# Kernel optimization log

Measured on AMD Instinct MI355X. Metric: run time of the kernel, lower is better.

## Reference

```python
import jax, jax.numpy as jnp
import numpy as np

N_NODES = 10000
N_EDGES = 160000
D = 512
DROPOUT_P = 0.5
NEG_SLOPE = 0.25


def setup_inputs() -> dict:
    key = jax.random.key(0)
    ks = jax.random.split(key, 8)
    H = jax.random.normal(ks[0], (N_NODES, D), dtype=jnp.float32)
    rows = jax.random.randint(ks[1], (N_EDGES,), 0, N_NODES)
    cols = jax.random.randint(ks[2], (N_EDGES,), 0, N_NODES)
    vals = jax.random.uniform(ks[3], (N_EDGES,), dtype=jnp.float32)
    # xavier-normal-ish weights, zero bias (matches torch init)
    std = float(np.sqrt(2.0 / (D + D)))
    W1 = jax.random.normal(ks[4], (D, D), dtype=jnp.float32) * std
    b1 = jnp.zeros((D,), dtype=jnp.float32)
    W2 = jax.random.normal(ks[5], (D, D), dtype=jnp.float32) * std
    b2 = jnp.zeros((D,), dtype=jnp.float32)
    return {"H": H, "rows": rows, "cols": cols, "vals": vals,
            "W1": W1, "b1": b1, "W2": W2, "b2": b2}


def _spmm(rows, cols, vals, dense):
    # sparse [N,N] @ dense [N,D] via gather + segment-sum
    gathered = vals[:, None] * dense[cols]          # [E, D]
    return jax.ops.segment_sum(gathered, rows, num_segments=N_NODES)


def _leaky_relu(x):
    return jnp.where(x >= 0, x, NEG_SLOPE * x)


def reference(H, rows, cols, vals, W1, b1, W2, b2):
    # layer 1: dense GEMM -> SpMM -> bias -> leaky_relu -> dropout(training=True)
    h = _spmm(rows, cols, vals, H @ W1) + b1
    h = _leaky_relu(h)
    keep = jax.random.bernoulli(jax.random.key(42), 1.0 - DROPOUT_P, h.shape)
    h = jnp.where(keep, h / (1.0 - DROPOUT_P), 0.0)
    # layer 2
    h = _spmm(rows, cols, vals, h @ W2) + b2
    return _leaky_relu(h)
```

## Files before the change

kernel.cpp:

```cpp
#include <hip/hip_runtime.h>
#include <stdint.h>

#define N_NODES 10000
#define M_PAD   10112
#define N_EDGES 160000
#define DIM     512
#define N_ELEMS 5120000
#define NEG_SLOPE 0.25f
#define ELL_W   64

typedef short          short8   __attribute__((ext_vector_type(8)));
typedef unsigned short ushort8v __attribute__((ext_vector_type(8)));
typedef __bf16         bf16x8   __attribute__((ext_vector_type(8)));
typedef float          f32x4    __attribute__((ext_vector_type(4)));

__device__ __forceinline__ unsigned short f2bf(float f) {
    uint32_t u = __builtin_bit_cast(uint32_t, f);
    uint32_t r = (u + 0x7fffu + ((u >> 16) & 1u)) >> 16;
    return (unsigned short)r;
}
__device__ __forceinline__ float b2f(unsigned short u) {
    return __builtin_bit_cast(float, (uint32_t)u << 16);
}

__device__ __forceinline__ uint32_t rotl32(uint32_t x, uint32_t d) {
    return (x << d) | (x >> (32u - d));
}
__device__ __forceinline__ void threefry_42(uint32_t x0, uint32_t x1,
                                            uint32_t& o0, uint32_t& o1) {
    const uint32_t ks0 = 0u, ks1 = 42u, ks2 = 0x1BD11BDAu ^ 42u;
    x0 += ks0; x1 += ks1;
#define TF_R4(a,b,c,d) \
    x0 += x1; x1 = rotl32(x1,a); x1 ^= x0; \
    x0 += x1; x1 = rotl32(x1,b); x1 ^= x0; \
    x0 += x1; x1 = rotl32(x1,c); x1 ^= x0; \
    x0 += x1; x1 = rotl32(x1,d); x1 ^= x0;
    TF_R4(13,15,26,6);  x0 += ks1; x1 += ks2 + 1u;
    TF_R4(17,29,16,24); x0 += ks2; x1 += ks0 + 2u;
    TF_R4(13,15,26,6);  x0 += ks0; x1 += ks1 + 3u;
    TF_R4(17,29,16,24); x0 += ks1; x1 += ks2 + 4u;
    TF_R4(13,15,26,6);  x0 += ks2; x1 += ks0 + 5u;
#undef TF_R4
    o0 = x0; o1 = x1;
}

#define CONV_BLKS 5000
#define TR_BLKS   64
#define EZ_BLKS   1250
#define ZERO_BLKS 10

__device__ __forceinline__ void transpose_tile(const float* __restrict__ W,
                                               unsigned short* __restrict__ WT,
                                               int tile, float (*ts)[65]) {
    int k0 = (tile & 7) * 64, n0 = (tile >> 3) * 64;
    int tx = threadIdx.x & 15, ty = threadIdx.x >> 4;
    #pragma unroll
    for (int i = 0; i < 4; ++i) {
        int k = i * 16 + ty;
        float4 v = *(const float4*)&W[(size_t)(k0 + k) * DIM + n0 + tx * 4];
        ts[k][tx * 4 + 0] = v.x; ts[k][tx * 4 + 1] = v.y;
        ts[k][tx * 4 + 2] = v.z; ts[k][tx * 4 + 3] = v.w;
    }
    __syncthreads();
    #pragma unroll
    for (int i = 0; i < 4; ++i) {
        int n = i * 16 + ty;
        ushort4 o;
        o.x = f2bf(ts[tx * 4 + 0][n]); o.y = f2bf(ts[tx * 4 + 1][n]);
        o.z = f2bf(ts[tx * 4 + 2][n]); o.w = f2bf(ts[tx * 4 + 3][n]);
        *(ushort4*)&WT[(size_t)(n0 + n) * DIM + k0 + tx * 4] = o;
    }
}

__global__ __launch_bounds__(256)
void prep_kernel(const float* __restrict__ H, const float* __restrict__ W1,
                 const float* __restrict__ W2, unsigned short* __restrict__ Abf,
                 unsigned short* __restrict__ WT1, unsigned short* __restrict__ WT2,
                 int4* __restrict__ epack4, int* __restrict__ deg) {
    __shared__ float ts[64][65];
    int b = blockIdx.x;
    if (b < CONV_BLKS) {
        int i = b * 256 + threadIdx.x;
        float4 v = ((const float4*)H)[i];
        ushort4 o;
        o.x = f2bf(v.x); o.y = f2bf(v.y); o.z = f2bf(v.z); o.w = f2bf(v.w);
        ((ushort4*)Abf)[i] = o;
    } else if (b < CONV_BLKS + TR_BLKS) {
        transpose_tile(W1, WT1, b - CONV_BLKS, ts);
    } else if (b < CONV_BLKS + 2 * TR_BLKS) {
        transpose_tile(W2, WT2, b - CONV_BLKS - TR_BLKS, ts);
    } else if (b < CONV_BLKS + 2 * TR_BLKS + EZ_BLKS) {
        int i = (b - CONV_BLKS - 2 * TR_BLKS) * 256 + threadIdx.x;
        epack4[i] = make_int4(0, 0, 0, 0);
    } else {
        int i = (b - CONV_BLKS - 2 * TR_BLKS - EZ_BLKS) * 1024 + threadIdx.x * 4;
        #pragma unroll
        for (int j = 0; j < 4; ++j)
            if (i + j < N_NODES) deg[i + j] = 0;
    }
}

__global__ void ell_scatter(const int* __restrict__ rows, const int* __restrict__ cols,
                            const float* __restrict__ vals, int* __restrict__ deg,
                            int2* __restrict__ epack) {
    int e = blockIdx.x * blockDim.x + threadIdx.x;
    if (e < N_EDGES) {
        int r = rows[e];
        int p = atomicAdd(&deg[r], 1);
        epack[(size_t)r * ELL_W + p] = make_int2(cols[e], __float_as_int(vals[e]));
    }
}

__global__ __launch_bounds__(256)
void mfma_gemm(const unsigned short* __restrict__ A, const unsigned short* __restrict__ BT,
               unsigned short* __restrict__ C, int M) {
    __shared__ short8 As[1024];
    __shared__ short8 Bs[1024];
    int tid  = threadIdx.x;
    int wid  = tid >> 6, lane = tid & 63;
    int bm   = blockIdx.x * 128;
    int bn   = blockIdx.y * 128;
    int wm   = (wid >> 1) * 64, wn = (wid & 1) * 64;

    f32x4 acc[4][4] = {};
    int srow = lane >> 3;
    int sslot = lane & 7;

    for (int k0 = 0; k0 < DIM; k0 += 64) {
        #pragma unroll
        for (int c = 0; c < 4; ++c) {
            int chunk = wid * 4 + c;
            int r  = chunk * 8 + srow;
            int ks = sslot ^ (r & 7);
            const unsigned short* ga = A  + (size_t)(bm + r) * DIM + k0 + ks * 8;
            const unsigned short* gb = BT + (size_t)(bn + r) * DIM + k0 + ks * 8;
            __builtin_amdgcn_global_load_lds(
                (const __attribute__((address_space(1))) void*)ga,
                (__attribute__((address_space(3))) void*)&As[chunk * 64], 16, 0, 0);
            __builtin_amdgcn_global_load_lds(
                (const __attribute__((address_space(1))) void*)gb,
                (__attribute__((address_space(3))) void*)&Bs[chunk * 64], 16, 0, 0);
        }
        __syncthreads();

        int lrow = lane & 15;
        int kgrp = lane >> 4;
        #pragma unroll
        for (int ks = 0; ks < 2; ++ks) {
            short8 af[4], bfr[4];
            #pragma unroll
            for (int i = 0; i < 4; ++i) {
                int r = wm + i * 16 + lrow;
                af[i]  = As[r * 8 + ((ks * 4 + kgrp) ^ (r & 7))];
                int n = wn + i * 16 + lrow;
                bfr[i] = Bs[n * 8 + ((ks * 4 + kgrp) ^ (n & 7))];
            }
            #pragma unroll
            for (int i = 0; i < 4; ++i)
                #pragma unroll
                for (int j = 0; j < 4; ++j)
                    acc[i][j] = __builtin_amdgcn_mfma_f32_16x16x32_bf16(
                        __builtin_bit_cast(bf16x8, af[i]),
                        __builtin_bit_cast(bf16x8, bfr[j]), acc[i][j], 0, 0, 0);
        }
        __syncthreads();
    }

    int crow = (lane >> 4) * 4;
    int ccol = lane & 15;
    #pragma unroll
    for (int i = 0; i < 4; ++i) {
        #pragma unroll
        for (int r = 0; r < 4; ++r) {
            int row = bm + wm + i * 16 + crow + r;
            if (row < M) {
                size_t base = (size_t)row * DIM + bn + wn + ccol;
                #pragma unroll
                for (int j = 0; j < 4; ++j)
                    C[base + j * 16] = f2bf(acc[i][j][r]);
            }
        }
    }
}

#define ACC2(v, U) \
    acc0 = fmaf(v, __builtin_bit_cast(float, (U) << 16), acc0); \
    acc1 = fmaf(v, __builtin_bit_cast(float, (U) & 0xffff0000u), acc1);

template <int LAYER>
__global__ __launch_bounds__(256)
void spmm_kernel(const unsigned short* __restrict__ X, const int* __restrict__ deg,
                 const int2* __restrict__ epack, const float* __restrict__ bias,
                 void* __restrict__ outp) {
    int b    = blockIdx.x;
    int q    = (b & 7) >> 1;
    int pi   = ((b >> 3) << 1) | (b & 1);
    int row  = pi * 4 + (threadIdx.x >> 6);
    int lane = threadIdx.x & 63;
    int d  = deg[row];
    int dp = (d + 7) & ~7;
    const int2* ep = epack + (size_t)row * ELL_W;
    const uint32_t* X2 = (const uint32_t*)X;
    uint32_t qoff = q * 64 + lane;

    float acc0 = 0.f, acc1 = 0.f;
    int base = 0;
    for (; base + 16 <= dp; base += 16) {
        int4 eA = *(const int4*)(ep + base);
        int4 eB = *(const int4*)(ep + base + 2);
        int4 eC = *(const int4*)(ep + base + 4);
        int4 eD = *(const int4*)(ep + base + 6);
        int4 eE = *(const int4*)(ep + base + 8);
        int4 eF = *(const int4*)(ep + base + 10);
        int4 eG = *(const int4*)(ep + base + 12);
        int4 eH = *(const int4*)(ep + base + 14);
        uint32_t x0 = X2[(size_t)eA.x * 256 + qoff];
        uint32_t x1 = X2[(size_t)eA.z * 256 + qoff];
        uint32_t x2 = X2[(size_t)eB.x * 256 + qoff];
        uint32_t x3 = X2[(size_t)eB.z * 256 + qoff];
        uint32_t x4 = X2[(size_t)eC.x * 256 + qoff];
        uint32_t x5 = X2[(size_t)eC.z * 256 + qoff];
        uint32_t x6 = X2[(size_t)eD.x * 256 + qoff];
        uint32_t x7 = X2[(size_t)eD.z * 256 + qoff];
        uint32_t x8 = X2[(size_t)eE.x * 256 + qoff];
        uint32_t x9 = X2[(size_t)eE.z * 256 + qoff];
        uint32_t xa = X2[(size_t)eF.x * 256 + qoff];
        uint32_t xb = X2[(size_t)eF.z * 256 + qoff];
        uint32_t xc = X2[(size_t)eG.x * 256 + qoff];
        uint32_t xd = X2[(size_t)eG.z * 256 + qoff];
        uint32_t xe = X2[(size_t)eH.x * 256 + qoff];
        uint32_t xf = X2[(size_t)eH.z * 256 + qoff];
        float v0 = __int_as_float(eA.y), v1 = __int_as_float(eA.w);
        float v2 = __int_as_float(eB.y), v3 = __int_as_float(eB.w);
        float v4 = __int_as_float(eC.y), v5 = __int_as_float(eC.w);
        float v6 = __int_as_float(eD.y), v7 = __int_as_float(eD.w);
        float v8 = __int_as_float(eE.y), v9 = __int_as_float(eE.w);
        float va = __int_as_float(eF.y), vb = __int_as_float(eF.w);
        float vc = __int_as_float(eG.y), vd = __int_as_float(eG.w);
        float ve = __int_as_float(eH.y), vf = __int_as_float(eH.w);
        ACC2(v0, x0) ACC2(v1, x1) ACC2(v2, x2) ACC2(v3, x3)
        ACC2(v4, x4) ACC2(v5, x5) ACC2(v6, x6) ACC2(v7, x7)
        ACC2(v8, x8) ACC2(v9, x9) ACC2(va, xa) ACC2(vb, xb)
        ACC2(vc, xc) ACC2(vd, xd) ACC2(ve, xe) ACC2(vf, xf)
    }
    if (base < dp) {
        int4 eA = *(const int4*)(ep + base);
        int4 eB = *(const int4*)(ep + base + 2);
        int4 eC = *(const int4*)(ep + base + 4);
        int4 eD = *(const int4*)(ep + base + 6);
        uint32_t x0 = X2[(size_t)eA.x * 256 + qoff];
        uint32_t x1 = X2[(size_t)eA.z * 256 + qoff];
        uint32_t x2 = X2[(size_t)eB.x * 256 + qoff];
        uint32_t x3 = X2[(size_t)eB.z * 256 + qoff];
        uint32_t x4 = X2[(size_t)eC.x * 256 + qoff];
        uint32_t x5 = X2[(size_t)eC.z * 256 + qoff];
        uint32_t x6 = X2[(size_t)eD.x * 256 + qoff];
        uint32_t x7 = X2[(size_t)eD.z * 256 + qoff];
        float v0 = __int_as_float(eA.y), v1 = __int_as_float(eA.w);
        float v2 = __int_as_float(eB.y), v3 = __int_as_float(eB.w);
        float v4 = __int_as_float(eC.y), v5 = __int_as_float(eC.w);
        float v6 = __int_as_float(eD.y), v7 = __int_as_float(eD.w);
        ACC2(v0, x0) ACC2(v1, x1) ACC2(v2, x2) ACC2(v3, x3)
        ACC2(v4, x4) ACC2(v5, x5) ACC2(v6, x6) ACC2(v7, x7)
    }

    float2 bi = ((const float2*)bias)[q * 64 + lane];
    float r0 = acc0 + bi.x, r1 = acc1 + bi.y;
    r0 = (r0 >= 0.f) ? r0 : NEG_SLOPE * r0;
    r1 = (r1 >= 0.f) ? r1 : NEG_SLOPE * r1;
    if (LAYER == 1) {
        uint32_t e0 = (uint32_t)row * DIM + q * 128 + lane * 2;
        uint32_t o0, o1;
        threefry_42(0u, e0, o0, o1);
        uint32_t bits0 = o0 ^ o1;
        threefry_42(0u, e0 + 1, o0, o1);
        uint32_t bits1 = o0 ^ o1;
        float w0 = ((int)bits0 >= 0) ? r0 * 2.0f : 0.0f;
        float w1 = ((int)bits1 >= 0) ? r1 * 2.0f : 0.0f;
        uint32_t o = (uint32_t)f2bf(w0) | ((uint32_t)f2bf(w1) << 16);
        ((uint32_t*)outp)[(size_t)row * 256 + q * 64 + lane] = o;
    } else {
        float2 o = make_float2(r0, r1);
        ((float2*)outp)[(size_t)row * 256 + q * 64 + lane] = o;
    }
}

extern "C" void kernel_launch(void* const* d_in, const int* in_sizes, int n_in,
                              void* d_out, int out_size, void* d_ws, size_t ws_size,
                              hipStream_t stream) {
    const float* H    = (const float*)d_in[0];
    const int*   rows = (const int*)  d_in[1];
    const int*   cols = (const int*)  d_in[2];
    const float* vals = (const float*)d_in[3];
    const float* W1   = (const float*)d_in[4];
    const float* b1   = (const float*)d_in[5];
    const float* W2   = (const float*)d_in[6];
    const float* b2   = (const float*)d_in[7];
    float* out = (float*)d_out;

    char* ws = (char*)d_ws;
    size_t off = 0;
    auto alloc = [&](size_t bytes) -> void* {
        off = (off + 255) & ~(size_t)255;
        void* p = ws + off;
        off += bytes;
        return p;
    };
    int*  deg   = (int*) alloc((size_t)N_NODES * 4);
    int2* epack = (int2*)alloc((size_t)N_NODES * ELL_W * 8);
    unsigned short* WT1 = (unsigned short*)alloc((size_t)DIM * DIM * 2);
    unsigned short* WT2 = (unsigned short*)alloc((size_t)DIM * DIM * 2);
    unsigned short* Abf = (unsigned short*)alloc((size_t)M_PAD * DIM * 2);
    unsigned short* hbf = (unsigned short*)alloc((size_t)M_PAD * DIM * 2);
    unsigned short* Xbf = (unsigned short*)alloc((size_t)N_NODES * DIM * 2);

    int prep_blocks = CONV_BLKS + 2 * TR_BLKS + EZ_BLKS + ZERO_BLKS;
    prep_kernel<<<prep_blocks, 256, 0, stream>>>(H, W1, W2, Abf, WT1, WT2,
                                                 (int4*)epack, deg);
    ell_scatter<<<(N_EDGES + 255) / 256, 256, 0, stream>>>(rows, cols, vals, deg, epack);

    dim3 ggrid(M_PAD / 128, DIM / 128);
    mfma_gemm<<<ggrid, 256, 0, stream>>>(Abf, WT1, Xbf, N_NODES);
    spmm_kernel<1><<<N_NODES, 256, 0, stream>>>(Xbf, deg, epack, b1, hbf);
    mfma_gemm<<<ggrid, 256, 0, stream>>>(hbf, WT2, Xbf, N_NODES);
    spmm_kernel<2><<<N_NODES, 256, 0, stream>>>(Xbf, deg, epack, b2, out);
}
```

Baseline: 104.3 us.

## Assign SpMM work items per XCD via atomic queues for L2 locality

Replaces the static block-to-(row group, column quarter) mapping in the SpMM kernels with dynamic work fetching. Each block reads its XCC id from a hardware register and pulls items from one of four atomic counters, so blocks on the same XCD tend to process the same column quarter of X and keep that slice in their local L2. It falls back to the other queues once its own is exhausted. This costs one atomic plus a block-wide sync per block, and the counters live in the deg allocation, which the prep kernel now zeroes.

```diff
diff --git a/kernel.cpp b/kernel.cpp
--- a/kernel.cpp
+++ b/kernel.cpp
@@ -96,7 +96,7 @@
         int i = (b - CONV_BLKS - 2 * TR_BLKS - EZ_BLKS) * 1024 + threadIdx.x * 4;
         #pragma unroll
         for (int j = 0; j < 4; ++j)
-            if (i + j < N_NODES) deg[i + j] = 0;
+            if (i + j < N_NODES + 8) deg[i + j] = 0;
     }
 }
 
@@ -191,11 +191,25 @@
 __global__ __launch_bounds__(256)
 void spmm_kernel(const unsigned short* __restrict__ X, const int* __restrict__ deg,
                  const int2* __restrict__ epack, const float* __restrict__ bias,
-                 void* __restrict__ outp) {
-    int b    = blockIdx.x;
-    int q    = (b & 7) >> 1;
-    int pi   = ((b >> 3) << 1) | (b & 1);
-    int row  = pi * 4 + (threadIdx.x >> 6);
+                 void* __restrict__ outp, int* __restrict__ qcur) {
+    __shared__ int s_item;
+    if (threadIdx.x == 0) {
+        uint32_t xcc = __builtin_amdgcn_s_getreg(6164);
+        int q0 = (int)((xcc >> 1) & 3);
+        int it = -1;
+        #pragma unroll
+        for (int t = 0; t < 4; ++t) {
+            int qq = (q0 + t) & 3;
+            int i = atomicAdd(&qcur[qq], 1);
+            if (i < N_NODES / 4) { it = (i << 2) | qq; break; }
+        }
+        s_item = it;
+    }
+    __syncthreads();
+    int item = s_item;
+    if (item < 0) return;
+    int q    = item & 3;
+    int row  = (item >> 2) * 4 + (threadIdx.x >> 6);
     int lane = threadIdx.x & 63;
     int d  = deg[row];
     int dp = (d + 7) & ~7;
@@ -306,7 +320,9 @@
         off += bytes;
         return p;
     };
-    int*  deg   = (int*) alloc((size_t)N_NODES * 4);
+    int*  deg   = (int*) alloc((size_t)(N_NODES + 8) * 4);
+    int*  qcurA = deg + N_NODES;
+    int*  qcurB = deg + N_NODES + 4;
     int2* epack = (int2*)alloc((size_t)N_NODES * ELL_W * 8);
     unsigned short* WT1 = (unsigned short*)alloc((size_t)DIM * DIM * 2);
     unsigned short* WT2 = (unsigned short*)alloc((size_t)DIM * DIM * 2);
@@ -321,7 +337,7 @@
 
     dim3 ggrid(M_PAD / 128, DIM / 128);
     mfma_gemm<<<ggrid, 256, 0, stream>>>(Abf, WT1, Xbf, N_NODES);
-    spmm_kernel<1><<<N_NODES, 256, 0, stream>>>(Xbf, deg, epack, b1, hbf);
+    spmm_kernel<1><<<N_NODES, 256, 0, stream>>>(Xbf, deg, epack, b1, hbf, qcurA);
     mfma_gemm<<<ggrid, 256, 0, stream>>>(hbf, WT2, Xbf, N_NODES);
-    spmm_kernel<2><<<N_NODES, 256, 0, stream>>>(Xbf, deg, epack, b2, out);
-}
+    spmm_kernel<2><<<N_NODES, 256, 0, stream>>>(Xbf, deg, epack, b2, out, qcurB);
+}
```

Result: slower. 295.4 us (+183.2%).
